# Kernel optimization log

Measured on AMD Instinct MI355X. Metric: run time of the kernel, lower is better.

## Reference

```python
import jax, jax.numpy as jnp
import numpy as np

CIN = 128
COUT = 128
B = 8192
N_DIAG = 17
LENS = [9 - abs(i - 8) for i in range(N_DIAG)]  # [1,2,...,9,...,2,1]


def setup_inputs() -> dict:
    key = jax.random.key(0)
    ks = jax.random.split(key, 2 + N_DIAG)
    d = {
        "weights": jax.random.normal(ks[0], (N_DIAG, COUT, CIN), jnp.float32),
        "bias": jax.random.normal(ks[1], (N_DIAG, COUT), jnp.float32),
    }
    for i, L in enumerate(LENS):
        d[f"x{i}"] = jax.random.normal(ks[2 + i], (B, L, CIN), jnp.float32)
    return d


def _diag_idx(i):
    # board positions (r, c) on anti-diagonal r + c == i of a 9x9 board
    rs = np.arange(max(0, i - 8), min(8, i) + 1)
    cs = i - rs
    return rs, cs


def _forward(weights, bias, xs):
    b = xs[0].shape[0]
    out = jnp.zeros((b, 9, 9, weights.shape[1]), xs[0].dtype)
    for i, x in enumerate(xs):
        # per-diagonal linear transform: (B, L_i, Cin) @ (Cout, Cin)^T + bias
        y = jnp.einsum('blc,oc->blo', x, weights[i]) + bias[i]
        rs, cs = _diag_idx(i)  # static numpy indices -> jit-friendly scatter
        out = out.at[:, rs, cs, :].set(y)
    return out


def reference(weights, bias, x0, x1, x2, x3, x4, x5, x6, x7, x8, x9, x10, x11,
              x12, x13, x14, x15, x16):
    xs = (x0, x1, x2, x3, x4, x5, x6, x7, x8, x9, x10, x11, x12, x13, x14,
          x15, x16)
    return _forward(weights, bias, xs)
```

## Files before the change

### kernel.cpp

```cpp
#include <hip/hip_runtime.h>
#include <hip/hip_bf16.h>

typedef __attribute__((ext_vector_type(8))) short short8;
typedef __attribute__((ext_vector_type(4))) float f32x4;
typedef __attribute__((ext_vector_type(4))) unsigned int u32x4;

struct XPtrs { const float* p[17]; };
struct Bases { int v[18]; };

#define CPB 2

__device__ __forceinline__ unsigned short f2bf(float f) {
  unsigned u = __float_as_uint(f);
  return (unsigned short)((u + 0x7fffu + ((u >> 16) & 1u)) >> 16);
}

__global__ __launch_bounds__(1024) void convert_w_kernel(
    const float* __restrict__ W, unsigned short* __restrict__ ws) {
  const int tid = blockIdx.x * 1024 + threadIdx.x;
  const int d  = tid >> 11;
  const int s2 = tid & 2047;
  const int sg = s2 >> 7;
  const int n  = s2 & 127;
  const float* src = W + ((size_t)d * 128 + n) * 128 + sg * 8;
  float4 a = *(const float4*)(src);
  float4 b = *(const float4*)(src + 4);
  unsigned u0 = (unsigned)f2bf(a.x) | ((unsigned)f2bf(a.y) << 16);
  unsigned u1 = (unsigned)f2bf(a.z) | ((unsigned)f2bf(a.w) << 16);
  unsigned u2 = (unsigned)f2bf(b.x) | ((unsigned)f2bf(b.y) << 16);
  unsigned u3 = (unsigned)f2bf(b.z) | ((unsigned)f2bf(b.w) << 16);
  *(uint4*)(ws + (size_t)tid * 8) = make_uint4(u0, u1, u2, u3);
}

__device__ __forceinline__ unsigned pack_bf2(float lo, float hi) {
  unsigned rl = __float_as_uint(lo) + 0x8000u;
  unsigned rh = __float_as_uint(hi) + 0x8000u;
  return __builtin_amdgcn_perm(rh, rl, 0x07060302u);
}

__device__ __forceinline__ void issue_unit_loads(
    const float* __restrict__ x, int u, int wave, int lr, int lg,
    float4 (&pf)[8]) {
  const float* xr = x + ((size_t)(u * 64 + wave * 16 + lr)) * 128 + lg * 8;
#pragma unroll
  for (int s = 0; s < 4; ++s) {
    pf[2 * s]     = *(const float4*)(xr + s * 32);
    pf[2 * s + 1] = *(const float4*)(xr + s * 32 + 4);
  }
}

__device__ __forceinline__ void convert_unit(const float4 (&pf)[8],
                                             short8 (&xf)[4]) {
#pragma unroll
  for (int s = 0; s < 4; ++s) {
    float4 a0 = pf[2 * s], a1 = pf[2 * s + 1];
    u32x4 w;
    w.x = pack_bf2(a0.x, a0.y);
    w.y = pack_bf2(a0.z, a0.w);
    w.z = pack_bf2(a1.x, a1.y);
    w.w = pack_bf2(a1.z, a1.w);
    xf[s] = __builtin_bit_cast(short8, w);
  }
}

__device__ __forceinline__ void compute_store_unit(
    const short8 (&xf)[4], const unsigned short* __restrict__ wlds,
    const float* __restrict__ blds, int u, int wave, int lr, int lg,
    int L, int start, int d, float* __restrict__ out) {
  const int f = u * 64 + wave * 16 + lr;
  const unsigned b = (unsigned)f / (unsigned)L;
  const int l = f - (int)b * L;
  float* orow = out + (size_t)b * 10368 + (size_t)(start * 8 + d) * 128
                + (size_t)l * 1024 + lg * 4;
#pragma unroll
  for (int nb = 0; nb < 8; ++nb) {
    f32x4 acc = *(const f32x4*)&blds[nb * 16 + lg * 4];
#pragma unroll
    for (int s = 0; s < 4; ++s) {
      short8 wf = *(const short8*)
          &wlds[(size_t)((s * 4 + lg) * 128 + nb * 16 + lr) * 8];
      acc = __builtin_amdgcn_mfma_f32_16x16x32_bf16(wf, xf[s], acc, 0, 0, 0);
    }
    *(f32x4*)(orow + nb * 16) = acc;
  }
}

__global__ __launch_bounds__(256) void diag_linear_kernel(
    XPtrs xp, Bases bb, const unsigned short* __restrict__ wsrc,
    const float* __restrict__ bias, float* __restrict__ out) {
  const int bid = blockIdx.x;
  int d = 0;
#pragma unroll
  for (int i = 1; i < 17; ++i) d += (bid >= bb.v[i]) ? 1 : 0;
  const int L = 9 - ((d < 8) ? (8 - d) : (d - 8));
  const int start = (d > 8) ? (d - 8) : 0;
  const float* __restrict__ x = xp.p[d];
  const int u0 = (bid - bb.v[d]) * CPB;

  const int t = threadIdx.x;
  const int lane = t & 63;
  const int wave = t >> 6;
  const int lr = lane & 15;
  const int lg = lane >> 4;

  __shared__ unsigned short wlds[2048 * 8];
  __shared__ float blds[128];

  {
    const unsigned short* gw = wsrc + (size_t)d * 16384;
    typedef const __attribute__((address_space(1))) unsigned int* gas_u32;
    typedef __attribute__((address_space(3))) unsigned int* las_u32;
#pragma unroll
    for (int r = 0; r < 8; ++r) {
      const int slotbase = (wave * 8 + r) * 64;
      __builtin_amdgcn_global_load_lds(
          (gas_u32)(const void*)(gw + (size_t)(slotbase + lane) * 8),
          (las_u32)(void*)(wlds + (size_t)slotbase * 8),
          16, 0, 0);
    }
    if (t < 32) {
      __builtin_amdgcn_global_load_lds(
          (gas_u32)(const void*)(bias + d * 128 + t * 4),
          (las_u32)(void*)(blds), 16, 0, 0);
    }
  }

  float4 pA[8], pB[8];
  issue_unit_loads(x, u0,     wave, lr, lg, pA);
  issue_unit_loads(x, u0 + 1, wave, lr, lg, pB);

  asm volatile("s_waitcnt vmcnt(16)" ::: "memory");
  __builtin_amdgcn_s_barrier();
  __builtin_amdgcn_sched_barrier(0);

  {
    short8 xf[4];
    convert_unit(pA, xf);
    compute_store_unit(xf, wlds, blds, u0, wave, lr, lg, L, start, d, out);
  }
  {
    short8 xf[4];
    convert_unit(pB, xf);
    compute_store_unit(xf, wlds, blds, u0 + 1, wave, lr, lg, L, start, d, out);
  }
}

extern "C" void kernel_launch(void* const* d_in, const int* in_sizes, int n_in,
                              void* d_out, int out_size, void* d_ws, size_t ws_size,
                              hipStream_t stream) {
  const float* W = (const float*)d_in[0];
  const float* bias = (const float*)d_in[1];
  XPtrs xp;
  for (int i = 0; i < 17; ++i) xp.p[i] = (const float*)d_in[2 + i];
  float* out = (float*)d_out;
  unsigned short* ws = (unsigned short*)d_ws;

  Bases bb;
  int base = 0;
  for (int i = 0; i < 17; ++i) {
    bb.v[i] = base;
    int L = 9 - ((i < 8) ? (8 - i) : (i - 8));
    base += (128 * L) / CPB;
  }
  bb.v[17] = base;

  convert_w_kernel<<<34, 1024, 0, stream>>>(W, ws);
  diag_linear_kernel<<<base, 256, 0, stream>>>(xp, bb, ws, bias, out);
}
```

Baseline: 146.2 us.

## Split output channels across block pairs and halve rows per block

```diff
diff --git a/kernel.cpp b/kernel.cpp
--- a/kernel.cpp
+++ b/kernel.cpp
@@ -8,7 +8,7 @@
 struct XPtrs { const float* p[17]; };
 struct Bases { int v[18]; };
 
-#define CPB 2
+#define UROWS 32
 
 __device__ __forceinline__ unsigned short f2bf(float f) {
   unsigned u = __float_as_uint(f);
@@ -41,7 +41,7 @@
 __device__ __forceinline__ void issue_unit_loads(
     const float* __restrict__ x, int u, int wave, int lr, int lg,
     float4 (&pf)[8]) {
-  const float* xr = x + ((size_t)(u * 64 + wave * 16 + lr)) * 128 + lg * 8;
+  const float* xr = x + ((size_t)(u * UROWS + wave * 16 + lr)) * 128 + lg * 8;
 #pragma unroll
   for (int s = 0; s < 4; ++s) {
     pf[2 * s]     = *(const float4*)(xr + s * 32);
@@ -65,27 +65,27 @@
 
 __device__ __forceinline__ void compute_store_unit(
     const short8 (&xf)[4], const unsigned short* __restrict__ wlds,
-    const float* __restrict__ blds, int u, int wave, int lr, int lg,
+    const float* __restrict__ blds, int u, int ch, int wave, int lr, int lg,
     int L, int start, int d, float* __restrict__ out) {
-  const int f = u * 64 + wave * 16 + lr;
+  const int f = u * UROWS + wave * 16 + lr;
   const unsigned b = (unsigned)f / (unsigned)L;
   const int l = f - (int)b * L;
   float* orow = out + (size_t)b * 10368 + (size_t)(start * 8 + d) * 128
-                + (size_t)l * 1024 + lg * 4;
+                + (size_t)l * 1024 + ch * 64 + lg * 4;
 #pragma unroll
-  for (int nb = 0; nb < 8; ++nb) {
+  for (int nb = 0; nb < 4; ++nb) {
     f32x4 acc = *(const f32x4*)&blds[nb * 16 + lg * 4];
 #pragma unroll
     for (int s = 0; s < 4; ++s) {
       short8 wf = *(const short8*)
-          &wlds[(size_t)((s * 4 + lg) * 128 + nb * 16 + lr) * 8];
+          &wlds[(size_t)((s * 4 + lg) * 64 + nb * 16 + lr) * 8];
       acc = __builtin_amdgcn_mfma_f32_16x16x32_bf16(wf, xf[s], acc, 0, 0, 0);
     }
     *(f32x4*)(orow + nb * 16) = acc;
   }
 }
 
-__global__ __launch_bounds__(256) void diag_linear_kernel(
+__global__ __launch_bounds__(128) void diag_linear_kernel(
     XPtrs xp, Bases bb, const unsigned short* __restrict__ wsrc,
     const float* __restrict__ bias, float* __restrict__ out) {
   const int bid = blockIdx.x;
@@ -95,7 +95,9 @@
   const int L = 9 - ((d < 8) ? (8 - d) : (d - 8));
   const int start = (d > 8) ? (d - 8) : 0;
   const float* __restrict__ x = xp.p[d];
-  const int u0 = (bid - bb.v[d]) * CPB;
+  const int bl = bid - bb.v[d];
+  const int ch = bl & 1;
+  const int u0 = (bl >> 1) * 2;
 
   const int t = threadIdx.x;
   const int lane = t & 63;
@@ -103,8 +105,8 @@
   const int lr = lane & 15;
   const int lg = lane >> 4;
 
-  __shared__ unsigned short wlds[2048 * 8];
-  __shared__ float blds[128];
+  __shared__ unsigned short wlds[1024 * 8];
+  __shared__ float blds[64];
 
   {
     const unsigned short* gw = wsrc + (size_t)d * 16384;
@@ -112,15 +114,17 @@
     typedef __attribute__((address_space(3))) unsigned int* las_u32;
 #pragma unroll
     for (int r = 0; r < 8; ++r) {
-      const int slotbase = (wave * 8 + r) * 64;
+      const int sg = wave * 8 + r;
+      const int gslot = sg * 128 + ch * 64 + lane;
+      const int lslot = sg * 64;
       __builtin_amdgcn_global_load_lds(
-          (gas_u32)(const void*)(gw + (size_t)(slotbase + lane) * 8),
-          (las_u32)(void*)(wlds + (size_t)slotbase * 8),
+          (gas_u32)(const void*)(gw + (size_t)gslot * 8),
+          (las_u32)(void*)(wlds + (size_t)lslot * 8),
           16, 0, 0);
     }
-    if (t < 32) {
+    if (t < 16) {
       __builtin_amdgcn_global_load_lds(
-          (gas_u32)(const void*)(bias + d * 128 + t * 4),
+          (gas_u32)(const void*)(bias + d * 128 + ch * 64 + t * 4),
           (las_u32)(void*)(blds), 16, 0, 0);
     }
   }
@@ -136,12 +140,12 @@
   {
     short8 xf[4];
     convert_unit(pA, xf);
-    compute_store_unit(xf, wlds, blds, u0, wave, lr, lg, L, start, d, out);
+    compute_store_unit(xf, wlds, blds, u0, ch, wave, lr, lg, L, start, d, out);
   }
   {
     short8 xf[4];
     convert_unit(pB, xf);
-    compute_store_unit(xf, wlds, blds, u0 + 1, wave, lr, lg, L, start, d, out);
+    compute_store_unit(xf, wlds, blds, u0 + 1, ch, wave, lr, lg, L, start, d, out);
   }
 }
 
@@ -160,10 +164,10 @@
   for (int i = 0; i < 17; ++i) {
     bb.v[i] = base;
     int L = 9 - ((i < 8) ? (8 - i) : (i - 8));
-    base += (128 * L) / CPB;
+    base += 256 * L;
   }
   bb.v[17] = base;
 
   convert_w_kernel<<<34, 1024, 0, stream>>>(W, ws);
-  diag_linear_kernel<<<base, 256, 0, stream>>>(xp, bb, ws, bias, out);
+  diag_linear_kernel<<<base, 128, 0, stream>>>(xp, bb, ws, bias, out);
 }
```

Result: slower. 168.1 us (+15.0%).

## Process 128 rows per block with 8 waves instead of two 64-row units

Applied to the files above, without the earlier changes.

```diff
diff --git a/kernel.cpp b/kernel.cpp
--- a/kernel.cpp
+++ b/kernel.cpp
@@ -7,8 +7,6 @@
 
 struct XPtrs { const float* p[17]; };
 struct Bases { int v[18]; };
-
-#define CPB 2
 
 __device__ __forceinline__ unsigned short f2bf(float f) {
   unsigned u = __float_as_uint(f);
@@ -38,54 +36,7 @@
   return __builtin_amdgcn_perm(rh, rl, 0x07060302u);
 }
 
-__device__ __forceinline__ void issue_unit_loads(
-    const float* __restrict__ x, int u, int wave, int lr, int lg,
-    float4 (&pf)[8]) {
-  const float* xr = x + ((size_t)(u * 64 + wave * 16 + lr)) * 128 + lg * 8;
-#pragma unroll
-  for (int s = 0; s < 4; ++s) {
-    pf[2 * s]     = *(const float4*)(xr + s * 32);
-    pf[2 * s + 1] = *(const float4*)(xr + s * 32 + 4);
-  }
-}
-
-__device__ __forceinline__ void convert_unit(const float4 (&pf)[8],
-                                             short8 (&xf)[4]) {
-#pragma unroll
-  for (int s = 0; s < 4; ++s) {
-    float4 a0 = pf[2 * s], a1 = pf[2 * s + 1];
-    u32x4 w;
-    w.x = pack_bf2(a0.x, a0.y);
-    w.y = pack_bf2(a0.z, a0.w);
-    w.z = pack_bf2(a1.x, a1.y);
-    w.w = pack_bf2(a1.z, a1.w);
-    xf[s] = __builtin_bit_cast(short8, w);
-  }
-}
-
-__device__ __forceinline__ void compute_store_unit(
-    const short8 (&xf)[4], const unsigned short* __restrict__ wlds,
-    const float* __restrict__ blds, int u, int wave, int lr, int lg,
-    int L, int start, int d, float* __restrict__ out) {
-  const int f = u * 64 + wave * 16 + lr;
-  const unsigned b = (unsigned)f / (unsigned)L;
-  const int l = f - (int)b * L;
-  float* orow = out + (size_t)b * 10368 + (size_t)(start * 8 + d) * 128
-                + (size_t)l * 1024 + lg * 4;
-#pragma unroll
-  for (int nb = 0; nb < 8; ++nb) {
-    f32x4 acc = *(const f32x4*)&blds[nb * 16 + lg * 4];
-#pragma unroll
-    for (int s = 0; s < 4; ++s) {
-      short8 wf = *(const short8*)
-          &wlds[(size_t)((s * 4 + lg) * 128 + nb * 16 + lr) * 8];
-      acc = __builtin_amdgcn_mfma_f32_16x16x32_bf16(wf, xf[s], acc, 0, 0, 0);
-    }
-    *(f32x4*)(orow + nb * 16) = acc;
-  }
-}
-
-__global__ __launch_bounds__(256) void diag_linear_kernel(
+__global__ __launch_bounds__(512) void diag_linear_kernel(
     XPtrs xp, Bases bb, const unsigned short* __restrict__ wsrc,
     const float* __restrict__ bias, float* __restrict__ out) {
   const int bid = blockIdx.x;
@@ -95,7 +46,7 @@
   const int L = 9 - ((d < 8) ? (8 - d) : (d - 8));
   const int start = (d > 8) ? (d - 8) : 0;
   const float* __restrict__ x = xp.p[d];
-  const int u0 = (bid - bb.v[d]) * CPB;
+  const int u0 = bid - bb.v[d];
 
   const int t = threadIdx.x;
   const int lane = t & 63;
@@ -111,8 +62,8 @@
     typedef const __attribute__((address_space(1))) unsigned int* gas_u32;
     typedef __attribute__((address_space(3))) unsigned int* las_u32;
 #pragma unroll
-    for (int r = 0; r < 8; ++r) {
-      const int slotbase = (wave * 8 + r) * 64;
+    for (int r = 0; r < 4; ++r) {
+      const int slotbase = (wave * 4 + r) * 64;
       __builtin_amdgcn_global_load_lds(
           (gas_u32)(const void*)(gw + (size_t)(slotbase + lane) * 8),
           (las_u32)(void*)(wlds + (size_t)slotbase * 8),
@@ -124,24 +75,49 @@
           (las_u32)(void*)(blds), 16, 0, 0);
     }
   }
+  __builtin_amdgcn_sched_barrier(0);
 
-  float4 pA[8], pB[8];
-  issue_unit_loads(x, u0,     wave, lr, lg, pA);
-  issue_unit_loads(x, u0 + 1, wave, lr, lg, pB);
+  float4 pf[8];
+  {
+    const float* xr = x + ((size_t)(u0 * 128 + wave * 16 + lr)) * 128 + lg * 8;
+#pragma unroll
+    for (int s = 0; s < 4; ++s) {
+      pf[2 * s]     = *(const float4*)(xr + s * 32);
+      pf[2 * s + 1] = *(const float4*)(xr + s * 32 + 4);
+    }
+  }
 
-  asm volatile("s_waitcnt vmcnt(16)" ::: "memory");
+  asm volatile("s_waitcnt vmcnt(8)" ::: "memory");
   __builtin_amdgcn_s_barrier();
   __builtin_amdgcn_sched_barrier(0);
 
-  {
-    short8 xf[4];
-    convert_unit(pA, xf);
-    compute_store_unit(xf, wlds, blds, u0, wave, lr, lg, L, start, d, out);
+  short8 xf[4];
+#pragma unroll
+  for (int s = 0; s < 4; ++s) {
+    float4 a0 = pf[2 * s], a1 = pf[2 * s + 1];
+    u32x4 w;
+    w.x = pack_bf2(a0.x, a0.y);
+    w.y = pack_bf2(a0.z, a0.w);
+    w.z = pack_bf2(a1.x, a1.y);
+    w.w = pack_bf2(a1.z, a1.w);
+    xf[s] = __builtin_bit_cast(short8, w);
   }
-  {
-    short8 xf[4];
-    convert_unit(pB, xf);
-    compute_store_unit(xf, wlds, blds, u0 + 1, wave, lr, lg, L, start, d, out);
+
+  const int f = u0 * 128 + wave * 16 + lr;
+  const unsigned b = (unsigned)f / (unsigned)L;
+  const int l = f - (int)b * L;
+  float* orow = out + (size_t)b * 10368 + (size_t)(start * 8 + d) * 128
+                + (size_t)l * 1024 + lg * 4;
+#pragma unroll
+  for (int nb = 0; nb < 8; ++nb) {
+    f32x4 acc = *(const f32x4*)&blds[nb * 16 + lg * 4];
+#pragma unroll
+    for (int s = 0; s < 4; ++s) {
+      short8 wf = *(const short8*)
+          &wlds[(size_t)((s * 4 + lg) * 128 + nb * 16 + lr) * 8];
+      acc = __builtin_amdgcn_mfma_f32_16x16x32_bf16(wf, xf[s], acc, 0, 0, 0);
+    }
+    *(f32x4*)(orow + nb * 16) = acc;
   }
 }
 
@@ -160,10 +136,10 @@
   for (int i = 0; i < 17; ++i) {
     bb.v[i] = base;
     int L = 9 - ((i < 8) ? (8 - i) : (i - 8));
-    base += (128 * L) / CPB;
+    base += 64 * L;
   }
   bb.v[17] = base;
 
   convert_w_kernel<<<34, 1024, 0, stream>>>(W, ws);
-  diag_linear_kernel<<<base, 256, 0, stream>>>(xp, bb, ws, bias, out);
+  diag_linear_kernel<<<base, 512, 0, stream>>>(xp, bb, ws, bias, out);
 }
```

Result: no change. 146.2 us (+0.0%).
